# Optimization experiments

Measured on AMD Instinct MI355X. Metric: run time of the kernel, lower is better.

Reference implementation:

```python
import jax, jax.numpy as jnp
import numpy as np

# Static problem sizes
REC = [5, 3, 6, 2]          # agents per scene (record_len), sum = 16
LMAX = max(REC)              # max cav count per group (static for padding)
C, H, W = 256, 96, 288       # feature channels and BEV spatial dims


def setup_inputs() -> dict:
    key = jax.random.key(0)
    total = sum(REC)
    x = jax.random.normal(key, (total, C, H, W), dtype=jnp.float32)
    record_len = jnp.array(REC, dtype=jnp.int32)
    return {"x": x, "record_len": record_len}


def _att_fusion(x, record_len):
    # x: (sum_cav, C, H, W); record_len: (B,)
    B = record_len.shape[0]
    Cdim, Hh, Ww = x.shape[1], x.shape[2], x.shape[3]
    P = Hh * Ww
    scale = 1.0 / np.sqrt(Cdim)

    # Pad ragged groups to (B, LMAX): row index into x, clamped + masked
    offsets = jnp.concatenate([jnp.zeros((1,), record_len.dtype),
                               jnp.cumsum(record_len)[:-1]])
    l = jnp.arange(LMAX)
    mask = l[None, :] < record_len[:, None]                       # (B, L)
    idx = offsets[:, None] + jnp.minimum(l[None, :], record_len[:, None] - 1)
    xf = x[idx].reshape(B, LMAX, Cdim, P)                         # (B, L, C, P)

    # Only the ego row (token 0) of the per-pixel self-attention is kept,
    # so compute attention for that single query per spatial location.
    q = xf[:, 0]                                                  # (B, C, P)
    scores = jnp.einsum('bcp,blcp->blp', q, xf) * scale           # (B, L, P)
    scores = jnp.where(mask[:, :, None], scores, jnp.float32(-1e9))
    attn = jax.nn.softmax(scores, axis=1)                         # over agents
    out = jnp.einsum('blp,blcp->bcp', attn, xf)                   # (B, C, P)
    return out.reshape(B, Cdim, Hh, Ww)


def reference(x, record_len):
    return _att_fusion(x, record_len)
```

## Files before the change

### kernel.cpp

```cpp
#include <hip/hip_runtime.h>


#define CC 256
#define PP (96 * 288)
#define P4 (PP / 4)
#define LMAXC 6

template <int LEN>
__device__ __forceinline__ void att_body(
    const float4* __restrict__ xbase,
    float4* __restrict__ obase,
    float4 (&red)[LMAXC][8][32],
    float4 (&att)[LMAXC][32],
    int pxl, int grp, int tid)
{
    const size_t CP4 = (size_t)CC * P4;

    float4 s[LEN];
#pragma unroll
    for (int l = 0; l < LEN; ++l) s[l] = make_float4(0.f, 0.f, 0.f, 0.f);

#pragma unroll 4
    for (int ci = 0; ci < 32; ++ci) {
        const size_t o = (size_t)ci * P4;
        float4 x0 = xbase[o];
        s[0].x = fmaf(x0.x, x0.x, s[0].x);
        s[0].y = fmaf(x0.y, x0.y, s[0].y);
        s[0].z = fmaf(x0.z, x0.z, s[0].z);
        s[0].w = fmaf(x0.w, x0.w, s[0].w);
#pragma unroll
        for (int l = 1; l < LEN; ++l) {
            float4 xl = xbase[o + (size_t)l * CP4];
            s[l].x = fmaf(x0.x, xl.x, s[l].x);
            s[l].y = fmaf(x0.y, xl.y, s[l].y);
            s[l].z = fmaf(x0.z, xl.z, s[l].z);
            s[l].w = fmaf(x0.w, xl.w, s[l].w);
        }
    }

#pragma unroll
    for (int l = 0; l < LEN; ++l) red[l][grp][pxl] = s[l];
    __syncthreads();

    if (tid < 32) {
        float4 v[LEN];
#pragma unroll
        for (int l = 0; l < LEN; ++l) {
            float4 a = make_float4(0.f, 0.f, 0.f, 0.f);
#pragma unroll
            for (int g = 0; g < 8; ++g) {
                float4 r = red[l][g][tid];
                a.x += r.x; a.y += r.y; a.z += r.z; a.w += r.w;
            }
            v[l] = make_float4(a.x * 0.0625f, a.y * 0.0625f,
                               a.z * 0.0625f, a.w * 0.0625f);
        }
        float4 m = v[0];
#pragma unroll
        for (int l = 1; l < LEN; ++l) {
            m.x = fmaxf(m.x, v[l].x); m.y = fmaxf(m.y, v[l].y);
            m.z = fmaxf(m.z, v[l].z); m.w = fmaxf(m.w, v[l].w);
        }
        float4 sum = make_float4(0.f, 0.f, 0.f, 0.f);
#pragma unroll
        for (int l = 0; l < LEN; ++l) {
            v[l].x = __expf(v[l].x - m.x); sum.x += v[l].x;
            v[l].y = __expf(v[l].y - m.y); sum.y += v[l].y;
            v[l].z = __expf(v[l].z - m.z); sum.z += v[l].z;
            v[l].w = __expf(v[l].w - m.w); sum.w += v[l].w;
        }
        float4 inv = make_float4(1.f / sum.x, 1.f / sum.y,
                                 1.f / sum.z, 1.f / sum.w);
#pragma unroll
        for (int l = 0; l < LEN; ++l)
            att[l][tid] = make_float4(v[l].x * inv.x, v[l].y * inv.y,
                                      v[l].z * inv.z, v[l].w * inv.w);
    }
    __syncthreads();

    float4 a[LEN];
#pragma unroll
    for (int l = 0; l < LEN; ++l) a[l] = att[l][pxl];

#pragma unroll 4
    for (int ci = 0; ci < 32; ++ci) {
        const size_t o = (size_t)ci * P4;
        float4 x0 = xbase[o];
        float4 acc;
        acc.x = a[0].x * x0.x; acc.y = a[0].y * x0.y;
        acc.z = a[0].z * x0.z; acc.w = a[0].w * x0.w;
#pragma unroll
        for (int l = 1; l < LEN; ++l) {
            float4 xl = xbase[o + (size_t)l * CP4];
            acc.x = fmaf(a[l].x, xl.x, acc.x);
            acc.y = fmaf(a[l].y, xl.y, acc.y);
            acc.z = fmaf(a[l].z, xl.z, acc.z);
            acc.w = fmaf(a[l].w, xl.w, acc.w);
        }
        obase[o] = acc;
    }
}

__global__ __launch_bounds__(256) void attfusion_kernel(
    const float4* __restrict__ x, const int* __restrict__ rl,
    float4* __restrict__ out)
{
    __shared__ float4 red[LMAXC][8][32];
    __shared__ float4 att[LMAXC][32];

    const int tid  = threadIdx.x;
    const int pxl  = tid & 31;
    const int grp  = tid >> 5;
    const int tile = blockIdx.x;
    const int b    = blockIdx.y;
    const int px4  = tile * 32 + pxl;
    const int c0   = grp * 32;

    int off = 0;
    for (int i = 0; i < b; ++i) off += rl[i];
    int len = rl[b];
    if (len > LMAXC) len = LMAXC;
    if (len < 1)     len = 1;

    const size_t CP4 = (size_t)CC * P4;
    const float4* xbase = x   + (size_t)off * CP4 + (size_t)c0 * P4 + px4;
    float4*       obase = out + (size_t)b   * CP4 + (size_t)c0 * P4 + px4;

    switch (len) {
        case 1: att_body<1>(xbase, obase, red, att, pxl, grp, tid); break;
        case 2: att_body<2>(xbase, obase, red, att, pxl, grp, tid); break;
        case 3: att_body<3>(xbase, obase, red, att, pxl, grp, tid); break;
        case 4: att_body<4>(xbase, obase, red, att, pxl, grp, tid); break;
        case 5: att_body<5>(xbase, obase, red, att, pxl, grp, tid); break;
        default: att_body<6>(xbase, obase, red, att, pxl, grp, tid); break;
    }
}

extern "C" void kernel_launch(void* const* d_in, const int* in_sizes, int n_in,
                              void* d_out, int out_size, void* d_ws, size_t ws_size,
                              hipStream_t stream) {
    const float4* x  = (const float4*)d_in[0];
    const int*    rl = (const int*)d_in[1];
    float4*       out = (float4*)d_out;
    const int B = in_sizes[1];
    dim3 grid(P4 / 32, B);
    attfusion_kernel<<<grid, 256, 0, stream>>>(x, rl, out);
}
```

Baseline: 711.1 us.

## Hold per-thread channel slice in registers to read input once

Each thread now loads its 8 channels for all agents into registers once and reuses them for both the score and weighted-sum passes, eliminating the second global read of x. Tiles shrink to 8 float4 pixels with 32 channel groups, the score reduction becomes a two-stage shared-memory step, and the grid is flattened with the batch index interleaved. This trades high register pressure and narrower contiguous segments per wavefront for roughly halving DRAM input traffic.

```diff
diff --git a/kernel.cpp b/kernel.cpp
--- a/kernel.cpp
+++ b/kernel.cpp
@@ -5,32 +5,37 @@
 #define PP (96 * 288)
 #define P4 (PP / 4)
 #define LMAXC 6
+#define TPX 8
+#define NGRP 32
 
 template <int LEN>
 __device__ __forceinline__ void att_body(
     const float4* __restrict__ xbase,
     float4* __restrict__ obase,
-    float4 (&red)[LMAXC][8][32],
-    float4 (&att)[LMAXC][32],
+    float4 (&red)[LMAXC][NGRP][TPX],
+    float4 (&sc)[LMAXC][TPX],
+    float4 (&att)[LMAXC][TPX],
     int pxl, int grp, int tid)
 {
     const size_t CP4 = (size_t)CC * P4;
 
+    float4 xd[LEN][8];
+#pragma unroll
+    for (int ci = 0; ci < 8; ++ci) {
+#pragma unroll
+        for (int l = 0; l < LEN; ++l)
+            xd[l][ci] = xbase[(size_t)l * CP4 + (size_t)ci * P4];
+    }
+
     float4 s[LEN];
 #pragma unroll
     for (int l = 0; l < LEN; ++l) s[l] = make_float4(0.f, 0.f, 0.f, 0.f);
-
-#pragma unroll 4
-    for (int ci = 0; ci < 32; ++ci) {
-        const size_t o = (size_t)ci * P4;
-        float4 x0 = xbase[o];
-        s[0].x = fmaf(x0.x, x0.x, s[0].x);
-        s[0].y = fmaf(x0.y, x0.y, s[0].y);
-        s[0].z = fmaf(x0.z, x0.z, s[0].z);
-        s[0].w = fmaf(x0.w, x0.w, s[0].w);
 #pragma unroll
-        for (int l = 1; l < LEN; ++l) {
-            float4 xl = xbase[o + (size_t)l * CP4];
+    for (int ci = 0; ci < 8; ++ci) {
+        const float4 x0 = xd[0][ci];
+#pragma unroll
+        for (int l = 0; l < LEN; ++l) {
+            const float4 xl = xd[l][ci];
             s[l].x = fmaf(x0.x, xl.x, s[l].x);
             s[l].y = fmaf(x0.y, xl.y, s[l].y);
             s[l].z = fmaf(x0.z, xl.z, s[l].z);
@@ -42,19 +47,23 @@
     for (int l = 0; l < LEN; ++l) red[l][grp][pxl] = s[l];
     __syncthreads();
 
-    if (tid < 32) {
+    if (tid < 8 * LEN) {
+        const int l = tid >> 3, px = tid & 7;
+        float4 a = make_float4(0.f, 0.f, 0.f, 0.f);
+#pragma unroll
+        for (int g = 0; g < NGRP; ++g) {
+            const float4 r = red[l][g][px];
+            a.x += r.x; a.y += r.y; a.z += r.z; a.w += r.w;
+        }
+        sc[l][px] = make_float4(a.x * 0.0625f, a.y * 0.0625f,
+                                a.z * 0.0625f, a.w * 0.0625f);
+    }
+    __syncthreads();
+
+    if (tid < TPX) {
         float4 v[LEN];
 #pragma unroll
-        for (int l = 0; l < LEN; ++l) {
-            float4 a = make_float4(0.f, 0.f, 0.f, 0.f);
-#pragma unroll
-            for (int g = 0; g < 8; ++g) {
-                float4 r = red[l][g][tid];
-                a.x += r.x; a.y += r.y; a.z += r.z; a.w += r.w;
-            }
-            v[l] = make_float4(a.x * 0.0625f, a.y * 0.0625f,
-                               a.z * 0.0625f, a.w * 0.0625f);
-        }
+        for (int l = 0; l < LEN; ++l) v[l] = sc[l][tid];
         float4 m = v[0];
 #pragma unroll
         for (int l = 1; l < LEN; ++l) {
@@ -69,8 +78,8 @@
             v[l].z = __expf(v[l].z - m.z); sum.z += v[l].z;
             v[l].w = __expf(v[l].w - m.w); sum.w += v[l].w;
         }
-        float4 inv = make_float4(1.f / sum.x, 1.f / sum.y,
-                                 1.f / sum.z, 1.f / sum.w);
+        const float4 inv = make_float4(1.f / sum.x, 1.f / sum.y,
+                                       1.f / sum.z, 1.f / sum.w);
 #pragma unroll
         for (int l = 0; l < LEN; ++l)
             att[l][tid] = make_float4(v[l].x * inv.x, v[l].y * inv.y,
@@ -82,39 +91,39 @@
 #pragma unroll
     for (int l = 0; l < LEN; ++l) a[l] = att[l][pxl];
 
-#pragma unroll 4
-    for (int ci = 0; ci < 32; ++ci) {
-        const size_t o = (size_t)ci * P4;
-        float4 x0 = xbase[o];
+#pragma unroll
+    for (int ci = 0; ci < 8; ++ci) {
         float4 acc;
-        acc.x = a[0].x * x0.x; acc.y = a[0].y * x0.y;
-        acc.z = a[0].z * x0.z; acc.w = a[0].w * x0.w;
+        acc.x = a[0].x * xd[0][ci].x;
+        acc.y = a[0].y * xd[0][ci].y;
+        acc.z = a[0].z * xd[0][ci].z;
+        acc.w = a[0].w * xd[0][ci].w;
 #pragma unroll
         for (int l = 1; l < LEN; ++l) {
-            float4 xl = xbase[o + (size_t)l * CP4];
-            acc.x = fmaf(a[l].x, xl.x, acc.x);
-            acc.y = fmaf(a[l].y, xl.y, acc.y);
-            acc.z = fmaf(a[l].z, xl.z, acc.z);
-            acc.w = fmaf(a[l].w, xl.w, acc.w);
+            acc.x = fmaf(a[l].x, xd[l][ci].x, acc.x);
+            acc.y = fmaf(a[l].y, xd[l][ci].y, acc.y);
+            acc.z = fmaf(a[l].z, xd[l][ci].z, acc.z);
+            acc.w = fmaf(a[l].w, xd[l][ci].w, acc.w);
         }
-        obase[o] = acc;
+        obase[(size_t)ci * P4] = acc;
     }
 }
 
-__global__ __launch_bounds__(256) void attfusion_kernel(
+__global__ __launch_bounds__(256, 2) void attfusion_kernel(
     const float4* __restrict__ x, const int* __restrict__ rl,
-    float4* __restrict__ out)
+    float4* __restrict__ out, int B)
 {
-    __shared__ float4 red[LMAXC][8][32];
-    __shared__ float4 att[LMAXC][32];
+    __shared__ float4 red[LMAXC][NGRP][TPX];
+    __shared__ float4 sc[LMAXC][TPX];
+    __shared__ float4 att[LMAXC][TPX];
 
-    const int tid  = threadIdx.x;
-    const int pxl  = tid & 31;
-    const int grp  = tid >> 5;
-    const int tile = blockIdx.x;
-    const int b    = blockIdx.y;
-    const int px4  = tile * 32 + pxl;
-    const int c0   = grp * 32;
+    const int tid = threadIdx.x;
+    const int pxl = tid & 7;
+    const int grp = tid >> 3;
+
+    const unsigned bid  = blockIdx.x;
+    const int b    = bid % (unsigned)B;
+    const int tile = bid / (unsigned)B;
 
     int off = 0;
     for (int i = 0; i < b; ++i) off += rl[i];
@@ -123,26 +132,29 @@
     if (len < 1)     len = 1;
 
     const size_t CP4 = (size_t)CC * P4;
-    const float4* xbase = x   + (size_t)off * CP4 + (size_t)c0 * P4 + px4;
-    float4*       obase = out + (size_t)b   * CP4 + (size_t)c0 * P4 + px4;
+    const int c0 = grp * 8;
+    const float4* xbase = x   + (size_t)off * CP4 + (size_t)c0 * P4
+                              + (size_t)tile * TPX + pxl;
+    float4*       obase = out + (size_t)b   * CP4 + (size_t)c0 * P4
+                              + (size_t)tile * TPX + pxl;
 
     switch (len) {
-        case 1: att_body<1>(xbase, obase, red, att, pxl, grp, tid); break;
-        case 2: att_body<2>(xbase, obase, red, att, pxl, grp, tid); break;
-        case 3: att_body<3>(xbase, obase, red, att, pxl, grp, tid); break;
-        case 4: att_body<4>(xbase, obase, red, att, pxl, grp, tid); break;
-        case 5: att_body<5>(xbase, obase, red, att, pxl, grp, tid); break;
-        default: att_body<6>(xbase, obase, red, att, pxl, grp, tid); break;
+        case 1: att_body<1>(xbase, obase, red, sc, att, pxl, grp, tid); break;
+        case 2: att_body<2>(xbase, obase, red, sc, att, pxl, grp, tid); break;
+        case 3: att_body<3>(xbase, obase, red, sc, att, pxl, grp, tid); break;
+        case 4: att_body<4>(xbase, obase, red, sc, att, pxl, grp, tid); break;
+        case 5: att_body<5>(xbase, obase, red, sc, att, pxl, grp, tid); break;
+        default: att_body<6>(xbase, obase, red, sc, att, pxl, grp, tid); break;
     }
 }
 
 extern "C" void kernel_launch(void* const* d_in, const int* in_sizes, int n_in,
                               void* d_out, int out_size, void* d_ws, size_t ws_size,
                               hipStream_t stream) {
-    const float4* x  = (const float4*)d_in[0];
-    const int*    rl = (const int*)d_in[1];
+    const float4* x   = (const float4*)d_in[0];
+    const int*    rl  = (const int*)d_in[1];
     float4*       out = (float4*)d_out;
     const int B = in_sizes[1];
-    dim3 grid(P4 / 32, B);
-    attfusion_kernel<<<grid, 256, 0, stream>>>(x, rl, out);
+    dim3 grid((P4 / TPX) * B);
+    attfusion_kernel<<<grid, 256, 0, stream>>>(x, rl, out, B);
 }
```

Measured after the change: 644.1 us. 1.1x faster.
